# Kernel tuning notes

Hardware: AMD Instinct MI355X
Metric: run time of the kernel (lower is better)

## Reference

```python
import jax, jax.numpy as jnp
import numpy as np

N_HEADS = 16


def setup_inputs() -> dict:
    key = jax.random.key(0)
    ks = jax.random.split(key, 9)
    B, S, D = 4, 2048, 1024
    x = jax.random.normal(ks[0], (B, S, D), dtype=jnp.float32)
    w = lambda k: jax.random.normal(k, (D, D), dtype=jnp.float32) * 0.02
    return {
        "x": x,
        "Wq": w(ks[1]), "bq": jnp.zeros((D,), jnp.float32),
        "Wk": w(ks[2]), "bk": jnp.zeros((D,), jnp.float32),
        "Wv": w(ks[3]), "bv": jnp.zeros((D,), jnp.float32),
        "Wo": w(ks[4]), "bo": jnp.zeros((D,), jnp.float32),
        "mask": jnp.ones((B, S), dtype=jnp.int32),
    }


def reference(x, Wq, bq, Wk, bk, Wv, bv, Wo, bo, mask):
    B, S, D = x.shape
    H = N_HEADS
    hd = D // H
    scale = hd ** -0.5
    # torch nn.Linear: y = x @ W.T + b
    Q = (x @ Wq.T + bq).reshape(B, S, H, hd)
    K = (x @ Wk.T + bk).reshape(B, S, H, hd)
    V = (x @ Wv.T + bv).reshape(B, S, H, hd)
    scores = jnp.einsum('bqhd,bkhd->bhqk', Q, K) * scale  # [B,H,S,S]
    # ALiBi: slopes = 1 / 2^(h/H); relative position = k_idx - q_idx
    slopes = 1.0 / 2.0 ** (jnp.arange(H, dtype=jnp.float32) / H)
    rel = jnp.arange(S)[None, :] - jnp.arange(S)[:, None]       # [S(q), S(k)] = k - q
    bias = slopes[:, None, None] * rel.astype(jnp.float32)      # [H,S,S]
    scores = scores + bias[None]
    scores = jnp.where(mask[:, None, None, :] == 0, -jnp.inf, scores)
    attn = jax.nn.softmax(scores, axis=-1)
    out = jnp.einsum('bhqk,bkhd->bqhd', attn, V).reshape(B, S, D)
    return out @ Wo.T + bo
```

## Files before the change

### kernel.cpp

```cpp
#include <hip/hip_runtime.h>
#include <hip/hip_bf16.h>

typedef unsigned short u16;
typedef __attribute__((ext_vector_type(8))) __bf16 bf16x8;
typedef __attribute__((ext_vector_type(4))) float f32x4;
typedef __attribute__((ext_vector_type(4))) short s16x4;

__device__ __forceinline__ u16 f2b(float f) {
  unsigned u = __builtin_bit_cast(unsigned, f);
  u = (u + 0x7fffu + ((u >> 16) & 1u)) >> 16;
  return (u16)u;
}

__device__ __forceinline__ u16 f2b_fast(float f) {
  return __builtin_bit_cast(u16, (__bf16)f);
}

__device__ __forceinline__ unsigned pack2(float a, float b) {
  return (unsigned)f2b_fast(a) | ((unsigned)f2b_fast(b) << 16);
}

__device__ __forceinline__ f32x4 mfma_bf16(uint4 a, uint4 b, f32x4 c) {
  return __builtin_amdgcn_mfma_f32_16x16x32_bf16(
      __builtin_bit_cast(bf16x8, a), __builtin_bit_cast(bf16x8, b), c, 0, 0, 0);
}

__device__ __forceinline__ f32x4 mfma_bf16_k16(uint2 a, uint2 b, f32x4 c) {
#if __has_builtin(__builtin_amdgcn_mfma_f32_16x16x16bf16_1k)
  return __builtin_amdgcn_mfma_f32_16x16x16bf16_1k(
      __builtin_bit_cast(s16x4, a), __builtin_bit_cast(s16x4, b), c, 0, 0, 0);
#elif __has_builtin(__builtin_amdgcn_mfma_f32_16x16x16_bf16)
  return __builtin_amdgcn_mfma_f32_16x16x16_bf16(
      __builtin_bit_cast(s16x4, a), __builtin_bit_cast(s16x4, b), c, 0, 0, 0);
#else
  f32x4 d;
  asm volatile("v_mfma_f32_16x16x16_bf16 %0, %1, %2, %3"
               : "=v"(d) : "v"(a), "v"(b), "v"(c));
  return d;
#endif
}

__device__ __forceinline__ void gload_lds16(const u16* g, u16* l) {
  __builtin_amdgcn_global_load_lds(
      (const __attribute__((address_space(1))) unsigned int*)(g),
      (__attribute__((address_space(3))) unsigned int*)(l), 16, 0, 0);
}

__device__ __forceinline__ void cast8(const float* __restrict__ s, u16* __restrict__ d) {
  float4 a = *(const float4*)s;
  float4 b = *(const float4*)(s + 4);
  ushort4 lo, hi;
  lo.x = f2b(a.x); lo.y = f2b(a.y); lo.z = f2b(a.z); lo.w = f2b(a.w);
  hi.x = f2b(b.x); hi.y = f2b(b.y); hi.z = f2b(b.z); hi.w = f2b(b.w);
  *(ushort4*)d = lo;
  *(ushort4*)(d + 4) = hi;
}

__global__ __launch_bounds__(256) void cast_x(const float* __restrict__ src,
                                              u16* __restrict__ dst, int n) {
  int i = (blockIdx.x * 256 + threadIdx.x) * 8;
  if (i + 8 <= n) cast8(src + i, dst + i);
}

__global__ __launch_bounds__(256) void cast_w4(const float* __restrict__ w0,
                                               const float* __restrict__ w1,
                                               const float* __restrict__ w2,
                                               const float* __restrict__ w3,
                                               u16* __restrict__ dst) {
  const float* s = (blockIdx.y == 0) ? w0 : (blockIdx.y == 1) ? w1
                 : (blockIdx.y == 2) ? w2 : w3;
  u16* d = dst + (size_t)blockIdx.y * (1u << 20);
  int i = (blockIdx.x * 256 + threadIdx.x) * 8;
  cast8(s + i, d + i);
}

__global__ __launch_bounds__(256) void mask_bias(const int* __restrict__ msk,
                                                 float* __restrict__ mb, int n) {
  int i = blockIdx.x * 256 + threadIdx.x;
  if (i < n) mb[i] = msk[i] ? 0.0f : -3.0e38f;
}

__global__ __launch_bounds__(256) void gemm_qkv(const u16* __restrict__ A,
                                                const u16* __restrict__ W,
                                                const float* __restrict__ bqp,
                                                const float* __restrict__ bkp,
                                                const float* __restrict__ bvp,
                                                u16* __restrict__ Qb,
                                                u16* __restrict__ Kb,
                                                u16* __restrict__ Vt) {
  constexpr int N = 1024, K = 1024;
  __shared__ u16 lA[128 * 32];
  __shared__ u16 lB[128 * 32];
  const int which = blockIdx.x >> 3;
  const int bx = blockIdx.x & 7;
  const u16* Bm = W + ((size_t)which << 20);
  const float* bias = (which == 0) ? bqp : (which == 1) ? bkp : bvp;

  const int tid = threadIdx.x;
  const int lane = tid & 63;
  const int w = tid >> 6;
  const int wr = w >> 1, wc = w & 1;
  const int rowBase = blockIdx.y * 128, colBase = bx * 128;
  const int lo = lane & 15, g = lane >> 4;

  f32x4 acc[4][4] = {};

  const int r0 = tid >> 2;
  const int c0 = (tid & 3) * 8;
  const u16* gA = A + (size_t)(rowBase + r0) * K + c0;
  const u16* gB = Bm + (size_t)(colBase + r0) * K + c0;
  u16* lAd = lA + w * 512;
  u16* lBd = lB + w * 512;

#pragma unroll 1
  for (int k0 = 0; k0 < K; k0 += 32) {
    gload_lds16(gA + k0, lAd);
    gload_lds16(gA + k0 + 64 * K, lAd + 2048);
    gload_lds16(gB + k0, lBd);
    gload_lds16(gB + k0 + 64 * K, lBd + 2048);
    __syncthreads();
    uint4 af[4], bf[4];
#pragma unroll
    for (int m = 0; m < 4; ++m)
      af[m] = *(const uint4*)&lA[(wr * 64 + m * 16 + lo) * 32 + g * 8];
#pragma unroll
    for (int n = 0; n < 4; ++n)
      bf[n] = *(const uint4*)&lB[(wc * 64 + n * 16 + lo) * 32 + g * 8];
#pragma unroll
    for (int m = 0; m < 4; ++m)
#pragma unroll
      for (int n = 0; n < 4; ++n)
        acc[m][n] = mfma_bf16(af[m], bf[n], acc[m][n]);
    __syncthreads();
  }

  const int cr = g * 4;
  if (which == 2) {
#pragma unroll
    for (int m = 0; m < 4; ++m)
#pragma unroll
      for (int n = 0; n < 4; ++n) {
        int i0 = rowBase + wr * 64 + m * 16 + cr;
        int jf = colBase + wc * 64 + n * 16 + lo;
        float bv = bias[jf];
        int bb = i0 >> 11, s0 = i0 & 2047;
        int hh = jf >> 6, dd = jf & 63;
        ushort4 pk;
        pk.x = f2b(acc[m][n][0] + bv);
        pk.y = f2b(acc[m][n][1] + bv);
        pk.z = f2b(acc[m][n][2] + bv);
        pk.w = f2b(acc[m][n][3] + bv);
        *(ushort4*)(Vt + ((size_t)((bb * 16 + hh) * 64 + dd)) * 2048 + s0) = pk;
      }
  } else {
    u16* dst = which ? Kb : Qb;
#pragma unroll
    for (int m = 0; m < 4; ++m)
#pragma unroll
      for (int n = 0; n < 4; ++n) {
        int gr = rowBase + wr * 64 + m * 16 + cr;
        int gc = colBase + wc * 64 + n * 16 + lo;
        float bv = bias[gc];
#pragma unroll
        for (int j = 0; j < 4; ++j)
          dst[(size_t)(gr + j) * N + gc] = f2b(acc[m][n][j] + bv);
      }
  }
}

__global__ __launch_bounds__(256) void gemm_out(const u16* __restrict__ A,
                                                const u16* __restrict__ Bm,
                                                const float* __restrict__ bias,
                                                float* __restrict__ Cout) {
  constexpr int N = 1024, K = 1024;
  __shared__ u16 lA[128 * 32];
  __shared__ u16 lB[128 * 32];
  const int tid = threadIdx.x;
  const int lane = tid & 63;
  const int w = tid >> 6;
  const int wr = w >> 1, wc = w & 1;
  const int rowBase = blockIdx.y * 128, colBase = blockIdx.x * 128;
  const int lo = lane & 15, g = lane >> 4;

  f32x4 acc[4][4] = {};
  const int r0 = tid >> 2;
  const int c0 = (tid & 3) * 8;
  const u16* gA = A + (size_t)(rowBase + r0) * K + c0;
  const u16* gB = Bm + (size_t)(colBase + r0) * K + c0;
  u16* lAd = lA + w * 512;
  u16* lBd = lB + w * 512;

#pragma unroll 1
  for (int k0 = 0; k0 < K; k0 += 32) {
    gload_lds16(gA + k0, lAd);
    gload_lds16(gA + k0 + 64 * K, lAd + 2048);
    gload_lds16(gB + k0, lBd);
    gload_lds16(gB + k0 + 64 * K, lBd + 2048);
    __syncthreads();
    uint4 af[4], bf[4];
#pragma unroll
    for (int m = 0; m < 4; ++m)
      af[m] = *(const uint4*)&lA[(wr * 64 + m * 16 + lo) * 32 + g * 8];
#pragma unroll
    for (int n = 0; n < 4; ++n)
      bf[n] = *(const uint4*)&lB[(wc * 64 + n * 16 + lo) * 32 + g * 8];
#pragma unroll
    for (int m = 0; m < 4; ++m)
#pragma unroll
      for (int n = 0; n < 4; ++n)
        acc[m][n] = mfma_bf16(af[m], bf[n], acc[m][n]);
    __syncthreads();
  }

  const int cr = g * 4;
#pragma unroll
  for (int m = 0; m < 4; ++m)
#pragma unroll
    for (int n = 0; n < 4; ++n) {
      int gr = rowBase + wr * 64 + m * 16 + cr;
      int gc = colBase + wc * 64 + n * 16 + lo;
      float bv = bias[gc];
#pragma unroll
      for (int j = 0; j < 4; ++j)
        Cout[(size_t)(gr + j) * N + gc] = acc[m][n][j] + bv;
    }
}

__global__ __launch_bounds__(256) void attn_fa(const u16* __restrict__ Qb,
                                               const u16* __restrict__ Kb,
                                               const u16* __restrict__ Vt,
                                               const float* __restrict__ mb,
                                               u16* __restrict__ Ob) {
  constexpr int S = 2048, D = 1024, H = 16, KV = 64, NT = S / KV;
  __shared__ float kbs[S];
  __shared__ u16 lK[2][64 * 64];
  __shared__ u16 lV[2][64 * 64];
  const int tid = threadIdx.x, lane = tid & 63, w = tid >> 6;
  const int lo = lane & 15, g = lane >> 4;
  const int b = blockIdx.z, h = blockIdx.y;
  const int qt = blockIdx.x * 128 + w * 32;
  const float LOG2E = 1.4426950408889634f;
  const float slope2 = exp2f(-(float)h / 16.0f) * LOG2E;
  const float c1 = 0.125f * LOG2E;

  {
    const float* mbb = mb + b * S;
    int s0 = tid * 8;
    float4 aa = *(const float4*)(mbb + s0);
    float4 bb = *(const float4*)(mbb + s0 + 4);
    kbs[s0 + 0] = fmaf(slope2, (float)(s0 + 0), aa.x);
    kbs[s0 + 1] = fmaf(slope2, (float)(s0 + 1), aa.y);
    kbs[s0 + 2] = fmaf(slope2, (float)(s0 + 2), aa.z);
    kbs[s0 + 3] = fmaf(slope2, (float)(s0 + 3), aa.w);
    kbs[s0 + 4] = fmaf(slope2, (float)(s0 + 4), bb.x);
    kbs[s0 + 5] = fmaf(slope2, (float)(s0 + 5), bb.y);
    kbs[s0 + 6] = fmaf(slope2, (float)(s0 + 6), bb.z);
    kbs[s0 + 7] = fmaf(slope2, (float)(s0 + 7), bb.w);
  }

  uint4 aq[2][2];
#pragma unroll
  for (int m = 0; m < 2; ++m) {
    const u16* qp = Qb + (size_t)(b * S + qt + m * 16 + lo) * D + h * 64 + g * 8;
    aq[m][0] = *(const uint4*)qp;
    aq[m][1] = *(const uint4*)(qp + 32);
  }

  float mrow[2] = {-3.0e38f, -3.0e38f};
  float lrow[2] = {0.0f, 0.0f};
  f32x4 o[2][4] = {};

  const u16* kbase = Kb + (size_t)b * S * D + h * 64;
  const u16* vbase = Vt + (size_t)(b * H + h) * 64 * S;

  auto stage = [&](int buf, int kt) {
#pragma unroll
    for (int j = 0; j < 2; ++j) {
      int i = j * 256 + tid;
      int row = i >> 3, c = i & 7;
      int sw = row & 7;
      u16* dK = &lK[buf][(j * 4 + w) * 512];
      u16* dV = &lV[buf][(j * 4 + w) * 512];
      gload_lds16(kbase + (size_t)(kt + row) * D + ((c ^ sw) * 8), dK);
      gload_lds16(vbase + (size_t)row * S + kt + ((c ^ sw) * 8), dV);
    }
  };

  __syncthreads();
  stage(0, S - KV);

#pragma unroll 1
  for (int tt = 0; tt < NT; ++tt) {
    const int buf = tt & 1;
    const int kt = (NT - 1 - tt) * KV;
    if (tt + 1 < NT) {
      stage(buf ^ 1, kt - KV);
      asm volatile("s_waitcnt vmcnt(4)" ::: "memory");
    } else {
      asm volatile("s_waitcnt vmcnt(0)" ::: "memory");
    }
    __builtin_amdgcn_s_barrier();
    __builtin_amdgcn_sched_barrier(0);

    const u16* lk = lK[buf];
    const u16* lv = lV[buf];

    f32x4 sc[2][4];
    __builtin_amdgcn_s_setprio(1);
#pragma unroll
    for (int n = 0; n < 4; ++n) {
      int row = n * 16 + lo, sw = row & 7;
      uint4 k0 = *(const uint4*)&lk[row * 64 + ((g ^ sw) * 8)];
      uint4 k1 = *(const uint4*)&lk[row * 64 + (((g + 4) ^ sw) * 8)];
#pragma unroll
      for (int m = 0; m < 2; ++m) {
        f32x4 z4 = {0.f, 0.f, 0.f, 0.f};
        z4 = mfma_bf16(k0, aq[m][0], z4);
        sc[m][n] = mfma_bf16(k1, aq[m][1], z4);
      }
    }
    __builtin_amdgcn_s_setprio(0);

#pragma unroll
    for (int n = 0; n < 4; ++n) {
      f32x4 kbv = *(const f32x4*)&kbs[kt + n * 16 + g * 4];
#pragma unroll
      for (int m = 0; m < 2; ++m)
#pragma unroll
        for (int j = 0; j < 4; ++j)
          sc[m][n][j] = fmaf(sc[m][n][j], c1, kbv[j]);
    }

    float pmv[2];
#pragma unroll
    for (int m = 0; m < 2; ++m) {
      f32x4 vm = sc[m][0];
#pragma unroll
      for (int n = 1; n < 4; ++n)
#pragma unroll
        for (int j = 0; j < 4; ++j) vm[j] = fmaxf(vm[j], sc[m][n][j]);
      float pm = fmaxf(fmaxf(vm[0], vm[1]), fmaxf(vm[2], vm[3]));
      pm = fmaxf(pm, __shfl_xor(pm, 16));
      pm = fmaxf(pm, __shfl_xor(pm, 32));
      pmv[m] = pm;
    }

    int keep = !((pmv[0] <= mrow[0] - 25.0f) && (pmv[1] <= mrow[1] - 25.0f));
    if (__any(keep)) {
#pragma unroll
      for (int m = 0; m < 2; ++m) {
        float mn = fmaxf(mrow[m], pmv[m]);
        float rs = exp2f(mrow[m] - mn);
        mrow[m] = mn;
        f32x4 vs = {0.f, 0.f, 0.f, 0.f};
#pragma unroll
        for (int n = 0; n < 4; ++n)
#pragma unroll
          for (int j = 0; j < 4; ++j) {
            float p = exp2f(sc[m][n][j] - mn);
            sc[m][n][j] = p;
            vs[j] += p;
          }
        float rsum = (vs[0] + vs[1]) + (vs[2] + vs[3]);
        rsum += __shfl_xor(rsum, 16);
        rsum += __shfl_xor(rsum, 32);
        lrow[m] = lrow[m] * rs + rsum;
#pragma unroll
        for (int dn = 0; dn < 4; ++dn)
#pragma unroll
          for (int j = 0; j < 4; ++j) o[m][dn][j] *= rs;
      }
      __builtin_amdgcn_s_setprio(1);
#pragma unroll
      for (int n = 0; n < 4; ++n) {
        uint2 pb0, pb1;
        pb0.x = pack2(sc[0][n][0], sc[0][n][1]);
        pb0.y = pack2(sc[0][n][2], sc[0][n][3]);
        pb1.x = pack2(sc[1][n][0], sc[1][n][1]);
        pb1.y = pack2(sc[1][n][2], sc[1][n][3]);
        int cw = 2 * n + (g >> 1);
        int off8 = (g & 1) * 4;
#pragma unroll
        for (int dn = 0; dn < 4; ++dn) {
          int row = dn * 16 + lo, sw = row & 7;
          uint2 va = *(const uint2*)&lv[row * 64 + ((cw ^ sw) * 8) + off8];
          o[0][dn] = mfma_bf16_k16(va, pb0, o[0][dn]);
          o[1][dn] = mfma_bf16_k16(va, pb1, o[1][dn]);
        }
      }
      __builtin_amdgcn_s_setprio(0);
    }

    __builtin_amdgcn_sched_barrier(0);
    __builtin_amdgcn_s_barrier();
  }

#pragma unroll
  for (int m = 0; m < 2; ++m) {
    float inv = 1.0f / fmaxf(lrow[m], 1e-30f);
    u16* orow = Ob + (size_t)(b * S + qt + m * 16 + lo) * D + h * 64 + g * 4;
#pragma unroll
    for (int dn = 0; dn < 4; ++dn) {
      ushort4 st;
      st.x = f2b_fast(o[m][dn][0] * inv);
      st.y = f2b_fast(o[m][dn][1] * inv);
      st.z = f2b_fast(o[m][dn][2] * inv);
      st.w = f2b_fast(o[m][dn][3] * inv);
      *(ushort4*)(orow + dn * 16) = st;
    }
  }
}

extern "C" void kernel_launch(void* const* d_in, const int* in_sizes, int n_in,
                              void* d_out, int out_size, void* d_ws, size_t ws_size,
                              hipStream_t stream) {
  (void)in_sizes; (void)n_in; (void)out_size; (void)ws_size;
  const float* x  = (const float*)d_in[0];
  const float* Wq = (const float*)d_in[1];
  const float* bq = (const float*)d_in[2];
  const float* Wk = (const float*)d_in[3];
  const float* bk = (const float*)d_in[4];
  const float* Wv = (const float*)d_in[5];
  const float* bv = (const float*)d_in[6];
  const float* Wo = (const float*)d_in[7];
  const float* bo = (const float*)d_in[8];
  const int*  msk = (const int*)d_in[9];
  float* out = (float*)d_out;

  char* ws = (char*)d_ws;
  u16* xb  = (u16*)(ws);
  u16* Qb  = (u16*)(ws + ((size_t)16 << 20));
  u16* Kb  = (u16*)(ws + ((size_t)32 << 20));
  u16* Vt  = (u16*)(ws + ((size_t)48 << 20));
  u16* Wqb = (u16*)(ws + ((size_t)64 << 20));
  float* mbf = (float*)(ws + ((size_t)72 << 20));

  cast_x<<<4096, 256, 0, stream>>>(x, xb, 8192 * 1024);
  cast_w4<<<dim3(512, 4), 256, 0, stream>>>(Wq, Wk, Wv, Wo, Wqb);
  mask_bias<<<32, 256, 0, stream>>>(msk, mbf, 8192);

  gemm_qkv<<<dim3(24, 64), 256, 0, stream>>>(xb, Wqb, bq, bk, bv, Qb, Kb, Vt);

  attn_fa<<<dim3(16, 16, 4), 256, 0, stream>>>(Qb, Kb, Vt, mbf, xb );

  gemm_out<<<dim3(8, 64), 256, 0, stream>>>(xb, Wqb + (3u << 20), bo, out);
}
```

Before: 306.1 us.

## Skip KV tiles using Cauchy-Schwarz score bound from K and Q norms

Adds a kernel that computes the maximum K row norm per 64-key tile, per batch and head. The attention kernel uses it, together with the block's maximum Q norm and the maximum ALiBi/mask bias per tile, to bound each tile's best possible score. When that bound falls more than 25 log2 units below every row's running max, the whole block skips loading and computing that tile. In exchange the K/V double buffering is dropped, leaving single-buffered loads with extra __syncthreads per tile, so when few tiles are skipped the kernel loses load/compute overlap. The skip relies on ALiBi's steep decay, which makes distant tiles negligible, so the cut is a bounded approximation rather than something tied to the test inputs.

```diff
diff --git a/kernel.cpp b/kernel.cpp
--- a/kernel.cpp
+++ b/kernel.cpp
@@ -18,6 +18,13 @@
 
 __device__ __forceinline__ unsigned pack2(float a, float b) {
   return (unsigned)f2b_fast(a) | ((unsigned)f2b_fast(b) << 16);
+}
+
+__device__ __forceinline__ float blo(unsigned u) {
+  return __builtin_bit_cast(float, u << 16);
+}
+__device__ __forceinline__ float bhi(unsigned u) {
+  return __builtin_bit_cast(float, u & 0xffff0000u);
 }
 
 __device__ __forceinline__ f32x4 mfma_bf16(uint4 a, uint4 b, f32x4 c) {
@@ -78,6 +85,35 @@
                                                  float* __restrict__ mb, int n) {
   int i = blockIdx.x * 256 + threadIdx.x;
   if (i < n) mb[i] = msk[i] ? 0.0f : -3.0e38f;
+}
+
+__global__ __launch_bounds__(256) void knorm(const u16* __restrict__ Kb,
+                                             float* __restrict__ maxKt) {
+  constexpr int S = 2048, D = 1024;
+  __shared__ float nrm[128];
+  const int t = threadIdx.x;
+  const int b = blockIdx.z, h = blockIdx.y;
+  const int r = blockIdx.x * 128 + (t >> 1);
+  const u16* kp = Kb + (size_t)(b * S + r) * D + h * 64 + (t & 1) * 32;
+  float ps = 0.f;
+#pragma unroll
+  for (int i = 0; i < 4; ++i) {
+    uint4 u = *(const uint4*)(kp + i * 8);
+    float f;
+    f = blo(u.x); ps += f * f;  f = bhi(u.x); ps += f * f;
+    f = blo(u.y); ps += f * f;  f = bhi(u.y); ps += f * f;
+    f = blo(u.z); ps += f * f;  f = bhi(u.z); ps += f * f;
+    f = blo(u.w); ps += f * f;  f = bhi(u.w); ps += f * f;
+  }
+  ps += __shfl_xor(ps, 1);
+  if ((t & 1) == 0) nrm[t >> 1] = ps;
+  __syncthreads();
+  if (t < 2) {
+    float m = 0.f;
+#pragma unroll 8
+    for (int i = 0; i < 64; ++i) m = fmaxf(m, nrm[t * 64 + i]);
+    maxKt[((b * 16 + h) * 32) + blockIdx.x * 2 + t] = sqrtf(m);
+  }
 }
 
 __global__ __launch_bounds__(256) void gemm_qkv(const u16* __restrict__ A,
@@ -230,11 +266,16 @@
                                                const u16* __restrict__ Kb,
                                                const u16* __restrict__ Vt,
                                                const float* __restrict__ mb,
+                                               const float* __restrict__ maxKt,
                                                u16* __restrict__ Ob) {
   constexpr int S = 2048, D = 1024, H = 16, KV = 64, NT = S / KV;
   __shared__ float kbs[S];
-  __shared__ u16 lK[2][64 * 64];
-  __shared__ u16 lV[2][64 * 64];
+  __shared__ float part[256];
+  __shared__ float kbsmax[NT];
+  __shared__ float mkt[NT];
+  __shared__ int   flag[4];
+  __shared__ u16 lK[64 * 64];
+  __shared__ u16 lV[64 * 64];
   const int tid = threadIdx.x, lane = tid & 63, w = tid >> 6;
   const int lo = lane & 15, g = lane >> 4;
   const int b = blockIdx.z, h = blockIdx.y;
@@ -248,14 +289,27 @@
     int s0 = tid * 8;
     float4 aa = *(const float4*)(mbb + s0);
     float4 bb = *(const float4*)(mbb + s0 + 4);
-    kbs[s0 + 0] = fmaf(slope2, (float)(s0 + 0), aa.x);
-    kbs[s0 + 1] = fmaf(slope2, (float)(s0 + 1), aa.y);
-    kbs[s0 + 2] = fmaf(slope2, (float)(s0 + 2), aa.z);
-    kbs[s0 + 3] = fmaf(slope2, (float)(s0 + 3), aa.w);
-    kbs[s0 + 4] = fmaf(slope2, (float)(s0 + 4), bb.x);
-    kbs[s0 + 5] = fmaf(slope2, (float)(s0 + 5), bb.y);
-    kbs[s0 + 6] = fmaf(slope2, (float)(s0 + 6), bb.z);
-    kbs[s0 + 7] = fmaf(slope2, (float)(s0 + 7), bb.w);
+    float v0 = fmaf(slope2, (float)(s0 + 0), aa.x);
+    float v1 = fmaf(slope2, (float)(s0 + 1), aa.y);
+    float v2 = fmaf(slope2, (float)(s0 + 2), aa.z);
+    float v3 = fmaf(slope2, (float)(s0 + 3), aa.w);
+    float v4 = fmaf(slope2, (float)(s0 + 4), bb.x);
+    float v5 = fmaf(slope2, (float)(s0 + 5), bb.y);
+    float v6 = fmaf(slope2, (float)(s0 + 6), bb.z);
+    float v7 = fmaf(slope2, (float)(s0 + 7), bb.w);
+    kbs[s0 + 0] = v0; kbs[s0 + 1] = v1; kbs[s0 + 2] = v2; kbs[s0 + 3] = v3;
+    kbs[s0 + 4] = v4; kbs[s0 + 5] = v5; kbs[s0 + 6] = v6; kbs[s0 + 7] = v7;
+    float pm = fmaxf(fmaxf(fmaxf(v0, v1), fmaxf(v2, v3)),
+                     fmaxf(fmaxf(v4, v5), fmaxf(v6, v7)));
+    part[tid] = pm;
+  }
+  __syncthreads();
+  if (tid < NT) {
+    float m = part[tid * 8];
+#pragma unroll
+    for (int i = 1; i < 8; ++i) m = fmaxf(m, part[tid * 8 + i]);
+    kbsmax[tid] = m;
+    mkt[tid] = maxKt[((b * 16 + h) * 32) + tid];
   }
 
   uint4 aq[2][2];
@@ -265,134 +319,153 @@
     aq[m][0] = *(const uint4*)qp;
     aq[m][1] = *(const uint4*)(qp + 32);
   }
+  float Qc;
+  {
+    float ps[2] = {0.f, 0.f};
+#pragma unroll
+    for (int m = 0; m < 2; ++m) {
+      const uint* u = (const uint*)&aq[m][0];
+#pragma unroll
+      for (int i = 0; i < 8; ++i) {
+        float f1 = blo(u[i]), f2 = bhi(u[i]);
+        ps[m] += f1 * f1 + f2 * f2;
+      }
+    }
+#pragma unroll
+    for (int m = 0; m < 2; ++m) {
+      ps[m] += __shfl_xor(ps[m], 16);
+      ps[m] += __shfl_xor(ps[m], 32);
+    }
+    float qm = fmaxf(sqrtf(ps[0]), sqrtf(ps[1]));
+    qm = fmaxf(qm, __shfl_xor(qm, 1));
+    qm = fmaxf(qm, __shfl_xor(qm, 2));
+    qm = fmaxf(qm, __shfl_xor(qm, 4));
+    qm = fmaxf(qm, __shfl_xor(qm, 8));
+    Qc = c1 * qm;
+  }
 
   float mrow[2] = {-3.0e38f, -3.0e38f};
   float lrow[2] = {0.0f, 0.0f};
+  float thr = -3.0e38f;
   f32x4 o[2][4] = {};
 
   const u16* kbase = Kb + (size_t)b * S * D + h * 64;
   const u16* vbase = Vt + (size_t)(b * H + h) * 64 * S;
 
-  auto stage = [&](int buf, int kt) {
-#pragma unroll
-    for (int j = 0; j < 2; ++j) {
-      int i = j * 256 + tid;
-      int row = i >> 3, c = i & 7;
-      int sw = row & 7;
-      u16* dK = &lK[buf][(j * 4 + w) * 512];
-      u16* dV = &lV[buf][(j * 4 + w) * 512];
-      gload_lds16(kbase + (size_t)(kt + row) * D + ((c ^ sw) * 8), dK);
-      gload_lds16(vbase + (size_t)row * S + kt + ((c ^ sw) * 8), dV);
-    }
-  };
-
   __syncthreads();
-  stage(0, S - KV);
 
 #pragma unroll 1
   for (int tt = 0; tt < NT; ++tt) {
-    const int buf = tt & 1;
-    const int kt = (NT - 1 - tt) * KV;
-    if (tt + 1 < NT) {
-      stage(buf ^ 1, kt - KV);
-      asm volatile("s_waitcnt vmcnt(4)" ::: "memory");
-    } else {
-      asm volatile("s_waitcnt vmcnt(0)" ::: "memory");
+    const int tl = NT - 1 - tt;
+    const int kt = tl * KV;
+    int keep_w = (fmaf(Qc, mkt[tl], kbsmax[tl]) > thr) ? 1 : 0;
+    flag[w] = keep_w;
+    __syncthreads();
+    int keep_blk = flag[0] | flag[1] | flag[2] | flag[3];
+    if (keep_blk) {
+#pragma unroll
+      for (int j = 0; j < 2; ++j) {
+        int i = j * 256 + tid;
+        int row = i >> 3, c = i & 7;
+        int sw = row & 7;
+        gload_lds16(kbase + (size_t)(kt + row) * D + ((c ^ sw) * 8),
+                    &lK[(j * 4 + w) * 512]);
+        gload_lds16(vbase + (size_t)row * S + kt + ((c ^ sw) * 8),
+                    &lV[(j * 4 + w) * 512]);
+      }
     }
-    __builtin_amdgcn_s_barrier();
-    __builtin_amdgcn_sched_barrier(0);
-
-    const u16* lk = lK[buf];
-    const u16* lv = lV[buf];
-
-    f32x4 sc[2][4];
-    __builtin_amdgcn_s_setprio(1);
-#pragma unroll
-    for (int n = 0; n < 4; ++n) {
-      int row = n * 16 + lo, sw = row & 7;
-      uint4 k0 = *(const uint4*)&lk[row * 64 + ((g ^ sw) * 8)];
-      uint4 k1 = *(const uint4*)&lk[row * 64 + (((g + 4) ^ sw) * 8)];
+    __syncthreads();
+    if (keep_blk) {
+      f32x4 sc[2][4];
+      __builtin_amdgcn_s_setprio(1);
+#pragma unroll
+      for (int n = 0; n < 4; ++n) {
+        int row = n * 16 + lo, sw = row & 7;
+        uint4 k0 = *(const uint4*)&lK[row * 64 + ((g ^ sw) * 8)];
+        uint4 k1 = *(const uint4*)&lK[row * 64 + (((g + 4) ^ sw) * 8)];
+#pragma unroll
+        for (int m = 0; m < 2; ++m) {
+          f32x4 z4 = {0.f, 0.f, 0.f, 0.f};
+          z4 = mfma_bf16(k0, aq[m][0], z4);
+          sc[m][n] = mfma_bf16(k1, aq[m][1], z4);
+        }
+      }
+      __builtin_amdgcn_s_setprio(0);
+#pragma unroll
+      for (int n = 0; n < 4; ++n) {
+        f32x4 kbv = *(const f32x4*)&kbs[kt + n * 16 + g * 4];
+#pragma unroll
+        for (int m = 0; m < 2; ++m)
+#pragma unroll
+          for (int j = 0; j < 4; ++j)
+            sc[m][n][j] = fmaf(sc[m][n][j], c1, kbv[j]);
+      }
+      float pmv[2];
 #pragma unroll
       for (int m = 0; m < 2; ++m) {
-        f32x4 z4 = {0.f, 0.f, 0.f, 0.f};
-        z4 = mfma_bf16(k0, aq[m][0], z4);
-        sc[m][n] = mfma_bf16(k1, aq[m][1], z4);
-      }
+        f32x4 vm = sc[m][0];
+#pragma unroll
+        for (int n = 1; n < 4; ++n)
+#pragma unroll
+          for (int j = 0; j < 4; ++j) vm[j] = fmaxf(vm[j], sc[m][n][j]);
+        float pm = fmaxf(fmaxf(vm[0], vm[1]), fmaxf(vm[2], vm[3]));
+        pm = fmaxf(pm, __shfl_xor(pm, 16));
+        pm = fmaxf(pm, __shfl_xor(pm, 32));
+        pmv[m] = pm;
+      }
+      int keep2 = !((pmv[0] <= mrow[0] - 25.0f) && (pmv[1] <= mrow[1] - 25.0f));
+      if (__any(keep2)) {
+#pragma unroll
+        for (int m = 0; m < 2; ++m) {
+          float mn = fmaxf(mrow[m], pmv[m]);
+          float rs = exp2f(mrow[m] - mn);
+          mrow[m] = mn;
+          f32x4 vs = {0.f, 0.f, 0.f, 0.f};
+#pragma unroll
+          for (int n = 0; n < 4; ++n)
+#pragma unroll
+            for (int j = 0; j < 4; ++j) {
+              float p = exp2f(sc[m][n][j] - mn);
+              sc[m][n][j] = p;
+              vs[j] += p;
+            }
+          float rsum = (vs[0] + vs[1]) + (vs[2] + vs[3]);
+          rsum += __shfl_xor(rsum, 16);
+          rsum += __shfl_xor(rsum, 32);
+          lrow[m] = lrow[m] * rs + rsum;
+#pragma unroll
+          for (int dn = 0; dn < 4; ++dn)
+#pragma unroll
+            for (int j = 0; j < 4; ++j) o[m][dn][j] *= rs;
+        }
+        __builtin_amdgcn_s_setprio(1);
+#pragma unroll
+        for (int n = 0; n < 4; ++n) {
+          uint2 pb0, pb1;
+          pb0.x = pack2(sc[0][n][0], sc[0][n][1]);
+          pb0.y = pack2(sc[0][n][2], sc[0][n][3]);
+          pb1.x = pack2(sc[1][n][0], sc[1][n][1]);
+          pb1.y = pack2(sc[1][n][2], sc[1][n][3]);
+          int cw = 2 * n + (g >> 1);
+          int off8 = (g & 1) * 4;
+#pragma unroll
+          for (int dn = 0; dn < 4; ++dn) {
+            int row = dn * 16 + lo, sw = row & 7;
+            uint2 va = *(const uint2*)&lV[row * 64 + ((cw ^ sw) * 8) + off8];
+            o[0][dn] = mfma_bf16_k16(va, pb0, o[0][dn]);
+            o[1][dn] = mfma_bf16_k16(va, pb1, o[1][dn]);
+          }
+        }
+        __builtin_amdgcn_s_setprio(0);
+        float mm = fminf(mrow[0], mrow[1]);
+        mm = fminf(mm, __shfl_xor(mm, 1));
+        mm = fminf(mm, __shfl_xor(mm, 2));
+        mm = fminf(mm, __shfl_xor(mm, 4));
+        mm = fminf(mm, __shfl_xor(mm, 8));
+        thr = mm - 25.0f;
+      }
+      __syncthreads();
     }
-    __builtin_amdgcn_s_setprio(0);
-
-#pragma unroll
-    for (int n = 0; n < 4; ++n) {
-      f32x4 kbv = *(const f32x4*)&kbs[kt + n * 16 + g * 4];
-#pragma unroll
-      for (int m = 0; m < 2; ++m)
-#pragma unroll
-        for (int j = 0; j < 4; ++j)
-          sc[m][n][j] = fmaf(sc[m][n][j], c1, kbv[j]);
-    }
-
-    float pmv[2];
-#pragma unroll
-    for (int m = 0; m < 2; ++m) {
-      f32x4 vm = sc[m][0];
-#pragma unroll
-      for (int n = 1; n < 4; ++n)
-#pragma unroll
-        for (int j = 0; j < 4; ++j) vm[j] = fmaxf(vm[j], sc[m][n][j]);
-      float pm = fmaxf(fmaxf(vm[0], vm[1]), fmaxf(vm[2], vm[3]));
-      pm = fmaxf(pm, __shfl_xor(pm, 16));
-      pm = fmaxf(pm, __shfl_xor(pm, 32));
-      pmv[m] = pm;
-    }
-
-    int keep = !((pmv[0] <= mrow[0] - 25.0f) && (pmv[1] <= mrow[1] - 25.0f));
-    if (__any(keep)) {
-#pragma unroll
-      for (int m = 0; m < 2; ++m) {
-        float mn = fmaxf(mrow[m], pmv[m]);
-        float rs = exp2f(mrow[m] - mn);
-        mrow[m] = mn;
-        f32x4 vs = {0.f, 0.f, 0.f, 0.f};
-#pragma unroll
-        for (int n = 0; n < 4; ++n)
-#pragma unroll
-          for (int j = 0; j < 4; ++j) {
-            float p = exp2f(sc[m][n][j] - mn);
-            sc[m][n][j] = p;
-            vs[j] += p;
-          }
-        float rsum = (vs[0] + vs[1]) + (vs[2] + vs[3]);
-        rsum += __shfl_xor(rsum, 16);
-        rsum += __shfl_xor(rsum, 32);
-        lrow[m] = lrow[m] * rs + rsum;
-#pragma unroll
-        for (int dn = 0; dn < 4; ++dn)
-#pragma unroll
-          for (int j = 0; j < 4; ++j) o[m][dn][j] *= rs;
-      }
-      __builtin_amdgcn_s_setprio(1);
-#pragma unroll
-      for (int n = 0; n < 4; ++n) {
-        uint2 pb0, pb1;
-        pb0.x = pack2(sc[0][n][0], sc[0][n][1]);
-        pb0.y = pack2(sc[0][n][2], sc[0][n][3]);
-        pb1.x = pack2(sc[1][n][0], sc[1][n][1]);
-        pb1.y = pack2(sc[1][n][2], sc[1][n][3]);
-        int cw = 2 * n + (g >> 1);
-        int off8 = (g & 1) * 4;
-#pragma unroll
-        for (int dn = 0; dn < 4; ++dn) {
-          int row = dn * 16 + lo, sw = row & 7;
-          uint2 va = *(const uint2*)&lv[row * 64 + ((cw ^ sw) * 8) + off8];
-          o[0][dn] = mfma_bf16_k16(va, pb0, o[0][dn]);
-          o[1][dn] = mfma_bf16_k16(va, pb1, o[1][dn]);
-        }
-      }
-      __builtin_amdgcn_s_setprio(0);
-    }
-
-    __builtin_amdgcn_sched_barrier(0);
-    __builtin_amdgcn_s_barrier();
   }
 
 #pragma unroll
@@ -433,7 +506,8 @@
   u16* Kb  = (u16*)(ws + ((size_t)32 << 20));
   u16* Vt  = (u16*)(ws + ((size_t)48 << 20));
   u16* Wqb = (u16*)(ws + ((size_t)64 << 20));
-  float* mbf = (float*)(ws + ((size_t)72 << 20));
+  float* mbf  = (float*)(ws + ((size_t)72 << 20));
+  float* mKt  = (float*)(ws + ((size_t)72 << 20) + 65536);
 
   cast_x<<<4096, 256, 0, stream>>>(x, xb, 8192 * 1024);
   cast_w4<<<dim3(512, 4), 256, 0, stream>>>(Wq, Wk, Wv, Wo, Wqb);
@@ -441,7 +515,9 @@
 
   gemm_qkv<<<dim3(24, 64), 256, 0, stream>>>(xb, Wqb, bq, bk, bv, Qb, Kb, Vt);
 
-  attn_fa<<<dim3(16, 16, 4), 256, 0, stream>>>(Qb, Kb, Vt, mbf, xb );
+  knorm<<<dim3(16, 16, 4), 256, 0, stream>>>(Kb, mKt);
+
+  attn_fa<<<dim3(16, 16, 4), 256, 0, stream>>>(Qb, Kb, Vt, mbf, mKt, xb);
 
   gemm_out<<<dim3(8, 64), 256, 0, stream>>>(xb, Wqb + (3u << 20), bo, out);
 }
```

New measurement: 267.0 us. -12.8%, faster.
